# Performance work log

Measured on AMD Instinct MI355X. Metric: run time of the kernel, lower is better.

## Reference

```python
import jax, jax.numpy as jnp
import numpy as np

B, T, I, H, L = 8192, 256, 28, 10, 2


def setup_inputs() -> dict:
    key = jax.random.key(0)
    ks = jax.random.split(key, 10)
    s_ih0 = 1.0 / np.sqrt(H)
    return {
        "x": jax.random.normal(ks[0], (B, T, I), dtype=jnp.float32),
        "h0": jnp.zeros((L, B, H), dtype=jnp.float32),
        "W_ih_l0": jax.random.uniform(ks[1], (H, I), minval=-s_ih0, maxval=s_ih0),
        "W_hh_l0": jax.random.uniform(ks[2], (H, H), minval=-s_ih0, maxval=s_ih0),
        "b_ih_l0": jax.random.uniform(ks[3], (H,), minval=-s_ih0, maxval=s_ih0),
        "b_hh_l0": jax.random.uniform(ks[4], (H,), minval=-s_ih0, maxval=s_ih0),
        "W_ih_l1": jax.random.uniform(ks[5], (H, H), minval=-s_ih0, maxval=s_ih0),
        "W_hh_l1": jax.random.uniform(ks[6], (H, H), minval=-s_ih0, maxval=s_ih0),
        "b_ih_l1": jax.random.uniform(ks[7], (H,), minval=-s_ih0, maxval=s_ih0),
        "b_hh_l1": jax.random.uniform(ks[8], (H,), minval=-s_ih0, maxval=s_ih0),
    }


def reference(x, h0, W_ih_l0, W_hh_l0, b_ih_l0, b_hh_l0,
              W_ih_l1, W_hh_l1, b_ih_l1, b_hh_l1):
    # torch RNN (tanh): h_t = tanh(x_t @ W_ih^T + b_ih + h_{t-1} @ W_hh^T + b_hh)
    # Precompute layer-0 input projections for all timesteps (big GEMM up front).
    xw0 = jnp.einsum('bti,hi->tbh', x, W_ih_l0) + (b_ih_l0 + b_hh_l0)  # [T,B,H]
    b1 = b_ih_l1 + b_hh_l1

    def step(carry, xw0_t):
        h_0, h_1 = carry
        h_0 = jnp.tanh(xw0_t + h_0 @ W_hh_l0.T)
        h_1 = jnp.tanh(h_0 @ W_ih_l1.T + b1 + h_1 @ W_hh_l1.T)
        return (h_0, h_1), h_1

    (hT_0, hT_1), out_tbh = jax.lax.scan(step, (h0[0], h0[1]), xw0)
    output = jnp.transpose(out_tbh, (1, 0, 2))          # [B,T,H] (batch_first)
    h_final = jnp.stack([hT_0, hT_1], axis=0)           # [2,B,H]
    return output, h_final
```

## Files before the change

### kernel.cpp

```cpp
#include <hip/hip_runtime.h>

#define B_ 8192
#define T_ 256
#define I_ 28
#define H_ 10

#define OUT_MAIN (B_ * T_ * H_)
#define BH (B_ * H_)

__device__ __forceinline__ float fast_tanh(float x) {
    float e = __builtin_amdgcn_exp2f(x * 2.885390081777927f);
    return __builtin_fmaf(-2.0f, __builtin_amdgcn_rcpf(e + 1.0f), 1.0f);
}

__global__ __launch_bounds__(256) void rnn_k1(
        const float* __restrict__ x, const float* __restrict__ Wih0,
        const float* __restrict__ bih0, const float* __restrict__ bhh0,
        float* __restrict__ xw0) {
    __shared__ float Wl[H_ * I_];
    __shared__ float bl[H_];
    int tid = threadIdx.x;
    for (int i = tid; i < H_ * I_; i += 256) Wl[i] = Wih0[i];
    if (tid < H_) bl[tid] = bih0[tid] + bhh0[tid];
    __syncthreads();

    long row0 = ((long)blockIdx.x * 256 + tid) * 2;
    const float* xr = x + row0 * I_;
    float xa[I_], xb[I_];
#pragma unroll
    for (int i = 0; i < 7; i++) {
        float4 va = ((const float4*)xr)[i];
        float4 vb = ((const float4*)(xr + I_))[i];
        xa[4*i+0] = va.x; xa[4*i+1] = va.y; xa[4*i+2] = va.z; xa[4*i+3] = va.w;
        xb[4*i+0] = vb.x; xb[4*i+1] = vb.y; xb[4*i+2] = vb.z; xb[4*i+3] = vb.w;
    }
    float oa[H_], ob[H_];
#pragma unroll
    for (int u = 0; u < H_; u++) {
        float s0 = bl[u], s1 = bl[u];
#pragma unroll
        for (int i = 0; i < I_; i++) {
            float w = Wl[u * I_ + i];
            s0 = __builtin_fmaf(xa[i], w, s0);
            s1 = __builtin_fmaf(xb[i], w, s1);
        }
        oa[u] = s0; ob[u] = s1;
    }
    float* o = xw0 + row0 * H_;
#pragma unroll
    for (int i = 0; i < 5; i++) {
        ((float2*)o)[i]        = make_float2(oa[2*i], oa[2*i+1]);
        ((float2*)(o + H_))[i] = make_float2(ob[2*i], ob[2*i+1]);
    }
}


#define SWZ(v, imm) __int_as_float(__builtin_amdgcn_ds_swizzle(__float_as_int(v), (imm)))

__global__ __launch_bounds__(256) void rnn_k2(
        float* __restrict__ buf,
        const float* __restrict__ h0in,
        const float* __restrict__ Whh0, const float* __restrict__ Wih1,
        const float* __restrict__ Whh1,
        const float* __restrict__ bih1, const float* __restrict__ bhh1,
        float* __restrict__ hfin) {
    int id = blockIdx.x * 256 + threadIdx.x;
    int b = id >> 3;
    int j = id & 7;
    bool act = (j < 5);
    int u0 = act ? 2 * j : 0;
    int u1 = act ? 2 * j + 1 : 0;

    float wh0a[H_], wh0b[H_], wi1a[H_], wi1b[H_], wh1a[H_], wh1b[H_];
#pragma unroll
    for (int k = 0; k < H_; k++) {
        wh0a[k] = Whh0[u0 * H_ + k]; wh0b[k] = Whh0[u1 * H_ + k];
        wi1a[k] = Wih1[u0 * H_ + k]; wi1b[k] = Wih1[u1 * H_ + k];
        wh1a[k] = Whh1[u0 * H_ + k]; wh1b[k] = Whh1[u1 * H_ + k];
    }
    float bb0 = bih1[u0] + bhh1[u0];
    float bb1 = bih1[u1] + bhh1[u1];

    float h0[H_], h1[H_];
#pragma unroll
    for (int k = 0; k < H_; k++) {
        h0[k] = h0in[b * H_ + k];
        h1[k] = h0in[BH + b * H_ + k];
    }

    float* base = buf + (long)b * (T_ * H_);
    float2 xbuf[4];
#pragma unroll
    for (int q = 0; q < 4; q++)
        xbuf[q] = act ? *(const float2*)(base + q * H_ + u0) : make_float2(0.f, 0.f);

    for (int t = 0; t < T_; t += 4) {
#pragma unroll
        for (int q = 0; q < 4; q++) {
            int tc = t + q;
            float a0 = xbuf[q].x, a1 = xbuf[q].y;
            if (tc + 4 < T_ && act)
                xbuf[q] = *(const float2*)(base + (tc + 4) * H_ + u0);
#pragma unroll
            for (int k = 0; k < H_; k++) {
                a0 = __builtin_fmaf(h0[k], wh0a[k], a0);
                a1 = __builtin_fmaf(h0[k], wh0b[k], a1);
            }
            float n0 = fast_tanh(a0), n1 = fast_tanh(a1);
            h0[0] = SWZ(n0, 0x18); h0[1] = SWZ(n1, 0x18);
            h0[2] = SWZ(n0, 0x38); h0[3] = SWZ(n1, 0x38);
            h0[4] = SWZ(n0, 0x58); h0[5] = SWZ(n1, 0x58);
            h0[6] = SWZ(n0, 0x78); h0[7] = SWZ(n1, 0x78);
            h0[8] = SWZ(n0, 0x98); h0[9] = SWZ(n1, 0x98);
            float c0 = bb0, c1 = bb1;
#pragma unroll
            for (int k = 0; k < H_; k++) {
                c0 = __builtin_fmaf(h0[k], wi1a[k], c0);
                c1 = __builtin_fmaf(h0[k], wi1b[k], c1);
                c0 = __builtin_fmaf(h1[k], wh1a[k], c0);
                c1 = __builtin_fmaf(h1[k], wh1b[k], c1);
            }
            float m0 = fast_tanh(c0), m1 = fast_tanh(c1);
            if (act)
                *(float2*)(base + tc * H_ + u0) = make_float2(m0, m1);
            h1[0] = SWZ(m0, 0x18); h1[1] = SWZ(m1, 0x18);
            h1[2] = SWZ(m0, 0x38); h1[3] = SWZ(m1, 0x38);
            h1[4] = SWZ(m0, 0x58); h1[5] = SWZ(m1, 0x58);
            h1[6] = SWZ(m0, 0x78); h1[7] = SWZ(m1, 0x78);
            h1[8] = SWZ(m0, 0x98); h1[9] = SWZ(m1, 0x98);
        }
    }
    if (act) {
        *(float2*)(hfin + b * H_ + u0)      = make_float2(h0[u0], h0[u1]);
        *(float2*)(hfin + BH + b * H_ + u0) = make_float2(h1[u0], h1[u1]);
    }
}

extern "C" void kernel_launch(void* const* d_in, const int* in_sizes, int n_in,
                              void* d_out, int out_size, void* d_ws, size_t ws_size,
                              hipStream_t stream) {
    const float* x     = (const float*)d_in[0];
    const float* h0in  = (const float*)d_in[1];
    const float* Wih0  = (const float*)d_in[2];
    const float* Whh0  = (const float*)d_in[3];
    const float* bih0  = (const float*)d_in[4];
    const float* bhh0  = (const float*)d_in[5];
    const float* Wih1  = (const float*)d_in[6];
    const float* Whh1  = (const float*)d_in[7];
    const float* bih1  = (const float*)d_in[8];
    const float* bhh1  = (const float*)d_in[9];
    float* out = (float*)d_out;

    rnn_k1<<<dim3((B_ * T_) / 512), dim3(256), 0, stream>>>(x, Wih0, bih0, bhh0, out);
    rnn_k2<<<dim3(256), dim3(256), 0, stream>>>(out, h0in, Whh0, Wih1, Whh1,
                                                bih1, bhh1, out + OUT_MAIN);
}
```

Before: 168.7 us.

## Use one lane per hidden unit with DPP row-rotate ring matvec

The recurrent kernel now gives each batch row 16 lanes, one hidden unit per lane, instead of 8 lanes each holding two units. Hidden-state exchange goes through DPP row_ror rotations fused into the FMA chain, replacing ds_swizzle broadcasts. Weights are stored pre-rotated and zero-padded so each lane multiplies by the right weight. This doubles the thread count and grid size and shortens each thread's dependent chain, at the cost of 6 of every 16 lanes doing wasted work and 15 DPP movs per matvec.

```diff
diff --git a/kernel.cpp b/kernel.cpp
--- a/kernel.cpp
+++ b/kernel.cpp
@@ -55,7 +55,17 @@
 }
 
 
-#define SWZ(v, imm) __int_as_float(__builtin_amdgcn_ds_swizzle(__float_as_int(v), (imm)))
+template <int S>
+__device__ __forceinline__ float rotf(float v) {
+    return __int_as_float(__builtin_amdgcn_mov_dpp(
+        __float_as_int(v), 0x120 + S, 0xF, 0xF, true));
+}
+
+template <int S>
+__device__ __forceinline__ void ring16(float& a, float v, const float (&w)[16]) {
+    a = __builtin_fmaf(rotf<S>(v), w[S], a);
+    if constexpr (S < 15) ring16<S + 1>(a, v, w);
+}
 
 __global__ __launch_bounds__(256) void rnn_k2(
         float* __restrict__ buf,
@@ -65,74 +75,50 @@
         const float* __restrict__ bih1, const float* __restrict__ bhh1,
         float* __restrict__ hfin) {
     int id = blockIdx.x * 256 + threadIdx.x;
-    int b = id >> 3;
-    int j = id & 7;
-    bool act = (j < 5);
-    int u0 = act ? 2 * j : 0;
-    int u1 = act ? 2 * j + 1 : 0;
+    int b = id >> 4;
+    int j = id & 15;
+    bool act = (j < 10);
 
-    float wh0a[H_], wh0b[H_], wi1a[H_], wi1b[H_], wh1a[H_], wh1b[H_];
+    float w0[16], wi[16], wh[16];
 #pragma unroll
-    for (int k = 0; k < H_; k++) {
-        wh0a[k] = Whh0[u0 * H_ + k]; wh0b[k] = Whh0[u1 * H_ + k];
-        wi1a[k] = Wih1[u0 * H_ + k]; wi1b[k] = Wih1[u1 * H_ + k];
-        wh1a[k] = Whh1[u0 * H_ + k]; wh1b[k] = Whh1[u1 * H_ + k];
+    for (int s = 0; s < 16; s++) {
+        int k = (j - s) & 15;
+        bool ok = act && (k < 10);
+        w0[s] = ok ? Whh0[j * H_ + k] : 0.f;
+        wi[s] = ok ? Wih1[j * H_ + k] : 0.f;
+        wh[s] = ok ? Whh1[j * H_ + k] : 0.f;
     }
-    float bb0 = bih1[u0] + bhh1[u0];
-    float bb1 = bih1[u1] + bhh1[u1];
-
-    float h0[H_], h1[H_];
-#pragma unroll
-    for (int k = 0; k < H_; k++) {
-        h0[k] = h0in[b * H_ + k];
-        h1[k] = h0in[BH + b * H_ + k];
-    }
+    float bj  = act ? (bih1[j] + bhh1[j]) : 0.f;
+    float h0v = act ? h0in[b * H_ + j] : 0.f;
+    float h1v = act ? h0in[BH + b * H_ + j] : 0.f;
 
     float* base = buf + (long)b * (T_ * H_);
-    float2 xbuf[4];
+    float xb[4];
 #pragma unroll
-    for (int q = 0; q < 4; q++)
-        xbuf[q] = act ? *(const float2*)(base + q * H_ + u0) : make_float2(0.f, 0.f);
+    for (int q = 0; q < 4; q++) xb[q] = act ? base[q * H_ + j] : 0.f;
 
     for (int t = 0; t < T_; t += 4) {
 #pragma unroll
         for (int q = 0; q < 4; q++) {
             int tc = t + q;
-            float a0 = xbuf[q].x, a1 = xbuf[q].y;
-            if (tc + 4 < T_ && act)
-                xbuf[q] = *(const float2*)(base + (tc + 4) * H_ + u0);
-#pragma unroll
-            for (int k = 0; k < H_; k++) {
-                a0 = __builtin_fmaf(h0[k], wh0a[k], a0);
-                a1 = __builtin_fmaf(h0[k], wh0b[k], a1);
-            }
-            float n0 = fast_tanh(a0), n1 = fast_tanh(a1);
-            h0[0] = SWZ(n0, 0x18); h0[1] = SWZ(n1, 0x18);
-            h0[2] = SWZ(n0, 0x38); h0[3] = SWZ(n1, 0x38);
-            h0[4] = SWZ(n0, 0x58); h0[5] = SWZ(n1, 0x58);
-            h0[6] = SWZ(n0, 0x78); h0[7] = SWZ(n1, 0x78);
-            h0[8] = SWZ(n0, 0x98); h0[9] = SWZ(n1, 0x98);
-            float c0 = bb0, c1 = bb1;
-#pragma unroll
-            for (int k = 0; k < H_; k++) {
-                c0 = __builtin_fmaf(h0[k], wi1a[k], c0);
-                c1 = __builtin_fmaf(h0[k], wi1b[k], c1);
-                c0 = __builtin_fmaf(h1[k], wh1a[k], c0);
-                c1 = __builtin_fmaf(h1[k], wh1b[k], c1);
-            }
-            float m0 = fast_tanh(c0), m1 = fast_tanh(c1);
-            if (act)
-                *(float2*)(base + tc * H_ + u0) = make_float2(m0, m1);
-            h1[0] = SWZ(m0, 0x18); h1[1] = SWZ(m1, 0x18);
-            h1[2] = SWZ(m0, 0x38); h1[3] = SWZ(m1, 0x38);
-            h1[4] = SWZ(m0, 0x58); h1[5] = SWZ(m1, 0x58);
-            h1[6] = SWZ(m0, 0x78); h1[7] = SWZ(m1, 0x78);
-            h1[8] = SWZ(m0, 0x98); h1[9] = SWZ(m1, 0x98);
+            float a = xb[q];
+            if (tc + 4 < T_) xb[q] = act ? base[(tc + 4) * H_ + j] : 0.f;
+            a = __builtin_fmaf(h0v, w0[0], a);
+            ring16<1>(a, h0v, w0);
+            float h0n = fast_tanh(a);
+            float c = bj;
+            c = __builtin_fmaf(h0n, wi[0], c);
+            c = __builtin_fmaf(h1v, wh[0], c);
+            ring16<1>(c, h0n, wi);
+            ring16<1>(c, h1v, wh);
+            float h1n = fast_tanh(c);
+            if (act) base[tc * H_ + j] = h1n;
+            h0v = h0n; h1v = h1n;
         }
     }
     if (act) {
-        *(float2*)(hfin + b * H_ + u0)      = make_float2(h0[u0], h0[u1]);
-        *(float2*)(hfin + BH + b * H_ + u0) = make_float2(h1[u0], h1[u1]);
+        hfin[b * H_ + j]      = h0v;
+        hfin[BH + b * H_ + j] = h1v;
     }
 }
 
@@ -152,6 +138,6 @@
     float* out = (float*)d_out;
 
     rnn_k1<<<dim3((B_ * T_) / 512), dim3(256), 0, stream>>>(x, Wih0, bih0, bhh0, out);
-    rnn_k2<<<dim3(256), dim3(256), 0, stream>>>(out, h0in, Whh0, Wih1, Whh1,
+    rnn_k2<<<dim3(512), dim3(256), 0, stream>>>(out, h0in, Whh0, Wih1, Whh1,
                                                 bih1, bhh1, out + OUT_MAIN);
 }
```

Result: slower. 232.3 us (+37.7%).
